# Optimization experiments

Measured on AMD Instinct MI355X. Metric: run time of the kernel, lower is better.

## Reference

```python
import jax, jax.numpy as jnp
import numpy as np

B, C, H, W = 8, 256, 64, 64
DQK = C // 8  # 32
EPS = 1e-5  # BatchNorm eps


def _conv_bn_relu(x, w, b, g, beta, mean, var):
    # 1x1 conv == channel matmul; BN in inference form (running stats)
    y = jnp.einsum('oc,bchw->bohw', w, x) + b[None, :, None, None]
    scale = g / jnp.sqrt(var + EPS)
    y = (y - mean[None, :, None, None]) * scale[None, :, None, None] + beta[None, :, None, None]
    return jax.nn.relu(y)


def setup_inputs() -> dict:
    key = jax.random.key(0)
    ks = jax.random.split(key, 20)
    f32 = jnp.float32

    def rn(i, shape, s=0.05):
        return jax.random.normal(ks[i], shape, dtype=f32) * s

    inp = {
        'x': jax.random.normal(ks[0], (B, C, H, W), dtype=f32),
        # query branch (C -> C//8)
        'wq': rn(1, (DQK, C)), 'bq': rn(2, (DQK,)),
        'gq': 1.0 + rn(3, (DQK,)), 'betaq': rn(4, (DQK,)),
        'mq': rn(5, (DQK,)), 'vq': jnp.abs(1.0 + rn(6, (DQK,))),
        # key branch (C -> C//8)
        'wk': rn(7, (DQK, C)), 'bk': rn(8, (DQK,)),
        'gk': 1.0 + rn(9, (DQK,)), 'betak': rn(10, (DQK,)),
        'mk': rn(11, (DQK,)), 'vk': jnp.abs(1.0 + rn(12, (DQK,))),
        # value branch (C -> C)
        'wv': rn(13, (C, C)), 'bv': rn(14, (C,)),
        'gv': 1.0 + rn(15, (C,)), 'betav': rn(16, (C,)),
        'mv': rn(17, (C,)), 'vv': jnp.abs(1.0 + rn(18, (C,))),
        # learnable residual gate (torch init is 0; nonzero for meaningful grads)
        'gamma': jnp.array([0.5], dtype=f32),
    }
    return inp


def reference(x, wq, bq, gq, betaq, mq, vq,
              wk, bk, gk, betak, mk, vk,
              wv, bv, gv, betav, mv, vv, gamma):
    b, c, h, w = x.shape
    n = h * w
    q = _conv_bn_relu(x, wq, bq, gq, betaq, mq, vq).reshape(b, DQK, n)  # [B,D,N]
    k = _conv_bn_relu(x, wk, bk, gk, betak, mk, vk).reshape(b, DQK, n)  # [B,D,N]
    v = _conv_bn_relu(x, wv, bv, gv, betav, mv, vv).reshape(b, c, n)    # [B,C,N]
    # energy[b,i,j] = <q_i, k_j>, unscaled as in the original
    energy = jnp.einsum('bdi,bdj->bij', q, k)          # [B,N,N]
    attn = jax.nn.softmax(energy, axis=-1)             # softmax over keys j
    # out[b,c,i] = sum_j V[b,c,j] * A[b,i,j]  (bmm with attention^T)
    out = jnp.einsum('bcj,bij->bci', v, attn).reshape(b, c, h, w)
    return gamma.reshape(1, 1, 1, 1) * out + x
```

## Files before the change

### kernel.cpp

```cpp
#include <hip/hip_runtime.h>
#include <math.h>
#include <stdint.h>
#include <stddef.h>

#define NB 8
#define NC 256
#define NN 4096
#define BN_EPS 1e-5f

typedef unsigned short u16;
typedef __attribute__((ext_vector_type(4))) unsigned short u16x4;
typedef __attribute__((ext_vector_type(8))) short bf16x8;
typedef __attribute__((ext_vector_type(4))) float f32x4;

static __device__ __forceinline__ float4 ld4(const float* p) { return *(const float4*)p; }
static __device__ __forceinline__ void st4(float* p, float4 v) { *(float4*)p = v; }
static __device__ __forceinline__ u16 f2bf(float f) {
  uint32_t u = __float_as_uint(f);
  return (u16)((u + 0x7FFFu + ((u >> 16) & 1u)) >> 16);
}

__global__ __launch_bounds__(256) void qkv_fused(
    const float* __restrict__ x,
    const float* __restrict__ wq, const float* __restrict__ bq,
    const float* __restrict__ gq, const float* __restrict__ betaq,
    const float* __restrict__ mq, const float* __restrict__ vq,
    const float* __restrict__ wk, const float* __restrict__ bk,
    const float* __restrict__ gk, const float* __restrict__ betak,
    const float* __restrict__ mk, const float* __restrict__ vk,
    const float* __restrict__ wv, const float* __restrict__ bv,
    const float* __restrict__ gv, const float* __restrict__ betav,
    const float* __restrict__ mv, const float* __restrict__ vv,
    u16* __restrict__ q_bf, u16* __restrict__ k_bf, u16* __restrict__ v_bf)
{
  __shared__ __align__(16) float smem[8704];
  float* sX = smem;
  float* sW = smem + 4096;
  float* sT = smem;

  const int tid   = threadIdx.x;
  const int bx    = blockIdx.x;
  const int b     = bx & 7;
  const int rem   = bx >> 3;
  const int ntile = rem & 31;
  const int otile = rem >> 5;
  const int n0    = ntile * 128;
  const int o0    = otile * 64;

  const int to = tid >> 4;
  const int tn = tid & 15;

  float acc[4][2][4];
#pragma unroll
  for (int j = 0; j < 4; ++j)
#pragma unroll
    for (int r = 0; r < 2; ++r)
#pragma unroll
      for (int e = 0; e < 4; ++e) acc[j][r][e] = 0.f;

  const float* xb = x + (size_t)b * NC * NN + n0;

  for (int ch = 0; ch < 8; ++ch) {
    const int c0 = ch * 32;
#pragma unroll
    for (int p = 0; p < 4; ++p) {
      int f = p * 256 + tid;
      int row = f >> 5, col4 = f & 31;
      st4(sX + row * 128 + col4 * 4, ld4(xb + (size_t)(c0 + row) * NN + col4 * 4));
    }
#pragma unroll
    for (int p = 0; p < 2; ++p) {
      int f = p * 256 + tid;
      int row = f >> 3, col4 = f & 7;
      int o = o0 + row;
      const float* wrow;
      if (o < 32)      wrow = wq + o * NC;
      else if (o < 64) wrow = wk + (o - 32) * NC;
      else             wrow = wv + (o - 64) * NC;
      st4(sW + row * 36 + col4 * 4, ld4(wrow + c0 + col4 * 4));
    }
    __syncthreads();

    for (int cc = 0; cc < 8; ++cc) {
      float wr[4][4];
#pragma unroll
      for (int j = 0; j < 4; ++j) {
        float4 t = ld4(sW + (to * 4 + j) * 36 + cc * 4);
        wr[j][0] = t.x; wr[j][1] = t.y; wr[j][2] = t.z; wr[j][3] = t.w;
      }
      float xr[4][2][4];
#pragma unroll
      for (int lc = 0; lc < 4; ++lc)
#pragma unroll
        for (int r = 0; r < 2; ++r) {
          float4 t = ld4(sX + (cc * 4 + lc) * 128 + tn * 4 + r * 64);
          xr[lc][r][0] = t.x; xr[lc][r][1] = t.y; xr[lc][r][2] = t.z; xr[lc][r][3] = t.w;
        }
#pragma unroll
      for (int j = 0; j < 4; ++j)
#pragma unroll
        for (int lc = 0; lc < 4; ++lc)
#pragma unroll
          for (int r = 0; r < 2; ++r)
#pragma unroll
            for (int e = 0; e < 4; ++e)
              acc[j][r][e] = fmaf(wr[j][lc], xr[lc][r][e], acc[j][r][e]);
    }
    __syncthreads();
  }

  if (otile == 0) {
#pragma unroll
    for (int j = 0; j < 4; ++j) {
      int o = to * 4 + j;
      float bias, g, beta, mean, var;
      if (o < 32) { int d = o;      bias = bq[d]; g = gq[d]; beta = betaq[d]; mean = mq[d]; var = vq[d]; }
      else        { int d = o - 32; bias = bk[d]; g = gk[d]; beta = betak[d]; mean = mk[d]; var = vk[d]; }
      float alpha = g * rsqrtf(var + BN_EPS);
      float delta = (bias - mean) * alpha + beta;
#pragma unroll
      for (int r = 0; r < 2; ++r)
#pragma unroll
        for (int e = 0; e < 4; ++e) {
          float y = fmaxf(fmaf(acc[j][r][e], alpha, delta), 0.f);
          int n = tn * 4 + r * 64 + e;
          sT[n * 68 + to * 4 + j] = y;
        }
    }
    __syncthreads();
    const size_t nrow = (size_t)b * NN + n0;
#pragma unroll
    for (int p = 0; p < 8; ++p) {
      int f = p * 256 + tid;
      int n = f >> 4, col4 = f & 15;
      float4 t = ld4(sT + n * 68 + col4 * 4);
      u16x4 h = { f2bf(t.x), f2bf(t.y), f2bf(t.z), f2bf(t.w) };
      if (col4 < 8) *(u16x4*)(q_bf + (nrow + n) * 32 + col4 * 4) = h;
      else          *(u16x4*)(k_bf + (nrow + n) * 32 + (col4 - 8) * 4) = h;
    }
  } else {
#pragma unroll
    for (int j = 0; j < 4; ++j) {
      int c = (otile - 1) * 64 + to * 4 + j;
      float alpha = gv[c] * rsqrtf(vv[c] + BN_EPS);
      float delta = (bv[c] - mv[c]) * alpha + betav[c];
#pragma unroll
      for (int r = 0; r < 2; ++r) {
        u16x4 h;
#pragma unroll
        for (int e = 0; e < 4; ++e)
          h[e] = f2bf(fmaxf(fmaf(acc[j][r][e], alpha, delta), 0.f));
        int n = n0 + tn * 4 + r * 64;
        *(u16x4*)(v_bf + ((size_t)b * NC + c) * NN + n) = h;
      }
    }
  }
}

__global__ __launch_bounds__(256, 4) void attn_mfma(
    const u16* __restrict__ q_bf, const u16* __restrict__ k_bf,
    const u16* __restrict__ v_bf, const float* __restrict__ x,
    const float* __restrict__ gamma, float* __restrict__ out)
{
  __shared__ u16 sP[4 * 32 * 64];

  const int tid = threadIdx.x;
  const int w   = tid >> 6;
  const int l   = tid & 63;
  const int xl  = l & 15;
  const int g   = l >> 4;
  const int b   = blockIdx.x & 7;
  const int rt  = blockIdx.x >> 3;
  const int i0  = rt * 32;

  u16* sPw = sP + w * 2048;

  const u16* qb = q_bf + ((size_t)b * NN + i0) * 32;
  const u16* kb = k_bf + (size_t)b * NN * 32;
  const u16* vb = v_bf + (size_t)b * NC * NN + (size_t)(w * 64) * NN;

  bf16x8 qf[2];
#pragma unroll
  for (int blk = 0; blk < 2; ++blk)
    qf[blk] = *(const bf16x8*)(qb + (size_t)(blk * 16 + xl) * 32 + 8 * g);

  f32x4 acc[2][4];
#pragma unroll
  for (int blk = 0; blk < 2; ++blk)
#pragma unroll
    for (int ct = 0; ct < 4; ++ct)
      acc[blk][ct] = (f32x4){0.f, 0.f, 0.f, 0.f};

  float mr[2][4], lr[2][4];
#pragma unroll
  for (int blk = 0; blk < 2; ++blk)
#pragma unroll
    for (int r = 0; r < 4; ++r) { mr[blk][r] = -INFINITY; lr[blk][r] = 0.f; }

  for (int jt64 = 0; jt64 < 64; ++jt64) {
    const int j0 = jt64 * 64;

    bf16x8 kf[4];
#pragma unroll
    for (int jb = 0; jb < 4; ++jb)
      kf[jb] = *(const bf16x8*)(kb + (size_t)(j0 + 16 * jb + xl) * 32 + 8 * g);

#pragma unroll
    for (int blk = 0; blk < 2; ++blk) {
      f32x4 s[4];
#pragma unroll
      for (int jb = 0; jb < 4; ++jb)
        s[jb] = __builtin_amdgcn_mfma_f32_16x16x32_bf16(
            qf[blk], kf[jb], (f32x4){0.f, 0.f, 0.f, 0.f}, 0, 0, 0);
      float pm[4];
#pragma unroll
      for (int r = 0; r < 4; ++r)
        pm[r] = fmaxf(fmaxf(s[0][r], s[1][r]), fmaxf(s[2][r], s[3][r]));
#pragma unroll
      for (int msk = 1; msk < 16; msk <<= 1)
#pragma unroll
        for (int r = 0; r < 4; ++r)
          pm[r] = fmaxf(pm[r], __shfl_xor(pm[r], msk));

      bool need = false;
#pragma unroll
      for (int r = 0; r < 4; ++r) need = need || (pm[r] > mr[blk][r]);
      if (__any(need)) {
        float sc[4];
#pragma unroll
        for (int r = 0; r < 4; ++r) {
          float mn = fmaxf(mr[blk][r], pm[r]);
          sc[r] = __expf(mr[blk][r] - mn);
          mr[blk][r] = mn;
          lr[blk][r] *= sc[r];
        }
#pragma unroll
        for (int ct = 0; ct < 4; ++ct)
#pragma unroll
          for (int r = 0; r < 4; ++r) acc[blk][ct][r] *= sc[r];
      }

      float ts[4] = {0.f, 0.f, 0.f, 0.f};
#pragma unroll
      for (int jb = 0; jb < 4; ++jb)
#pragma unroll
        for (int r = 0; r < 4; ++r) {
          float p = __expf(s[jb][r] - mr[blk][r]);
          ts[r] += p;
          int irow = blk * 16 + 4 * g + r;
          sPw[irow * 64 + ((16 * jb + xl) ^ ((irow & 7) << 3))] = f2bf(p);
        }
#pragma unroll
      for (int msk = 1; msk < 16; msk <<= 1)
#pragma unroll
        for (int r = 0; r < 4; ++r) ts[r] += __shfl_xor(ts[r], msk);
#pragma unroll
      for (int r = 0; r < 4; ++r) lr[blk][r] += ts[r];
    }

#pragma unroll
    for (int jt = 0; jt < 2; ++jt) {
      bf16x8 pf[2];
#pragma unroll
      for (int blk = 0; blk < 2; ++blk) {
        int irow = blk * 16 + xl;
        pf[blk] = *(const bf16x8*)(sPw + irow * 64 +
                                   ((jt * 32 + 8 * g) ^ ((irow & 7) << 3)));
      }
#pragma unroll
      for (int ct = 0; ct < 4; ++ct) {
        bf16x8 vf = *(const bf16x8*)(vb + (size_t)(ct * 16 + xl) * NN +
                                     j0 + jt * 32 + 8 * g);
        acc[0][ct] = __builtin_amdgcn_mfma_f32_16x16x32_bf16(pf[0], vf, acc[0][ct], 0, 0, 0);
        acc[1][ct] = __builtin_amdgcn_mfma_f32_16x16x32_bf16(pf[1], vf, acc[1][ct], 0, 0, 0);
      }
    }
  }

  float linv[2][4];
#pragma unroll
  for (int blk = 0; blk < 2; ++blk)
#pragma unroll
    for (int r = 0; r < 4; ++r) linv[blk][r] = 1.f / lr[blk][r];

  const float gm = gamma[0];
#pragma unroll
  for (int blk = 0; blk < 2; ++blk)
#pragma unroll
    for (int ct = 0; ct < 4; ++ct) {
      int c = w * 64 + ct * 16 + xl;
      size_t off = ((size_t)b * NC + c) * NN + i0 + blk * 16 + 4 * g;
      float4 xv = ld4(x + off);
      float4 o4;
      o4.x = fmaf(gm, acc[blk][ct][0] * linv[blk][0], xv.x);
      o4.y = fmaf(gm, acc[blk][ct][1] * linv[blk][1], xv.y);
      o4.z = fmaf(gm, acc[blk][ct][2] * linv[blk][2], xv.z);
      o4.w = fmaf(gm, acc[blk][ct][3] * linv[blk][3], xv.w);
      st4(out + off, o4);
    }
}

extern "C" void kernel_launch(void* const* d_in, const int* in_sizes, int n_in,
                              void* d_out, int out_size, void* d_ws, size_t ws_size,
                              hipStream_t stream) {
  const float* x     = (const float*)d_in[0];
  const float* wq    = (const float*)d_in[1];
  const float* bq    = (const float*)d_in[2];
  const float* gq    = (const float*)d_in[3];
  const float* betaq = (const float*)d_in[4];
  const float* mq    = (const float*)d_in[5];
  const float* vq    = (const float*)d_in[6];
  const float* wk    = (const float*)d_in[7];
  const float* bk    = (const float*)d_in[8];
  const float* gk    = (const float*)d_in[9];
  const float* betak = (const float*)d_in[10];
  const float* mk    = (const float*)d_in[11];
  const float* vk    = (const float*)d_in[12];
  const float* wv    = (const float*)d_in[13];
  const float* bv    = (const float*)d_in[14];
  const float* gv    = (const float*)d_in[15];
  const float* betav = (const float*)d_in[16];
  const float* mv    = (const float*)d_in[17];
  const float* vv    = (const float*)d_in[18];
  const float* gamma = (const float*)d_in[19];
  float* out = (float*)d_out;

  u16* q_bf = (u16*)d_ws;
  u16* k_bf = q_bf + (size_t)NB * NN * 32;
  u16* v_bf = k_bf + (size_t)NB * NN * 32;

  qkv_fused<<<dim3(1280), dim3(256), 0, stream>>>(
      x, wq, bq, gq, betaq, mq, vq,
      wk, bk, gk, betak, mk, vk,
      wv, bv, gv, betav, mv, vv,
      q_bf, k_bf, v_bf);

  attn_mfma<<<dim3(1024), dim3(256), 0, stream>>>(q_bf, k_bf, v_bf, x, gamma, out);
}
```

Measured before the change: 549.4 us.

## Split score and softmax work across waves and share row stats via LDS

Each of the four waves previously recomputed the full 32x64 QK^T tile and its exponentials. Now each wave computes only its own 16-key slice, writes it into a single shared P tile, and exchanges per-row max and sum partials through small LDS arrays, with two block barriers per key tile. Log2(e) is folded into the query BN scale so exp2f replaces __expf. The next key fragment and the V fragments are also loaded earlier to hide latency. In exchange, each iteration gains barrier and LDS traffic, and the last iteration prefetches key data past the end of the batch slice.

New measurement: 627.8 us. 1.14x slower.

```diff
diff --git a/kernel.cpp b/kernel.cpp
--- a/kernel.cpp
+++ b/kernel.cpp
@@ -7,6 +7,7 @@
 #define NC 256
 #define NN 4096
 #define BN_EPS 1e-5f
+#define LOG2E 1.44269504088896340736f
 
 typedef unsigned short u16;
 typedef __attribute__((ext_vector_type(4))) unsigned short u16x4;
@@ -118,6 +119,7 @@
       else        { int d = o - 32; bias = bk[d]; g = gk[d]; beta = betak[d]; mean = mk[d]; var = vk[d]; }
       float alpha = g * rsqrtf(var + BN_EPS);
       float delta = (bias - mean) * alpha + beta;
+      if (o < 32) { alpha *= LOG2E; delta *= LOG2E; }
 #pragma unroll
       for (int r = 0; r < 2; ++r)
 #pragma unroll
@@ -162,7 +164,9 @@
     const u16* __restrict__ v_bf, const float* __restrict__ x,
     const float* __restrict__ gamma, float* __restrict__ out)
 {
-  __shared__ u16 sP[4 * 32 * 64];
+  __shared__ u16 sP[32 * 64];
+  __shared__ float sMx[32 * 4];
+  __shared__ float sLx[32 * 4];
 
   const int tid = threadIdx.x;
   const int w   = tid >> 6;
@@ -173,16 +177,13 @@
   const int rt  = blockIdx.x >> 3;
   const int i0  = rt * 32;
 
-  u16* sPw = sP + w * 2048;
-
-  const u16* qb = q_bf + ((size_t)b * NN + i0) * 32;
-  const u16* kb = k_bf + (size_t)b * NN * 32;
-  const u16* vb = v_bf + (size_t)b * NC * NN + (size_t)(w * 64) * NN;
+  const u16* qb  = q_bf + ((size_t)b * NN + i0) * 32;
+  const u16* kb0 = k_bf + (size_t)b * NN * 32 + (size_t)(16 * w + xl) * 32 + 8 * g;
+  const u16* vb  = v_bf + ((size_t)b * NC + w * 64) * NN;
 
   bf16x8 qf[2];
-#pragma unroll
-  for (int blk = 0; blk < 2; ++blk)
-    qf[blk] = *(const bf16x8*)(qb + (size_t)(blk * 16 + xl) * 32 + 8 * g);
+  qf[0] = *(const bf16x8*)(qb + (size_t)xl * 32 + 8 * g);
+  qf[1] = *(const bf16x8*)(qb + (size_t)(16 + xl) * 32 + 8 * g);
 
   f32x4 acc[2][4];
 #pragma unroll
@@ -197,84 +198,121 @@
 #pragma unroll
     for (int r = 0; r < 4; ++r) { mr[blk][r] = -INFINITY; lr[blk][r] = 0.f; }
 
+  bf16x8 kf = *(const bf16x8*)kb0;
+
   for (int jt64 = 0; jt64 < 64; ++jt64) {
     const int j0 = jt64 * 64;
 
-    bf16x8 kf[4];
-#pragma unroll
-    for (int jb = 0; jb < 4; ++jb)
-      kf[jb] = *(const bf16x8*)(kb + (size_t)(j0 + 16 * jb + xl) * 32 + 8 * g);
-
-#pragma unroll
-    for (int blk = 0; blk < 2; ++blk) {
-      f32x4 s[4];
-#pragma unroll
-      for (int jb = 0; jb < 4; ++jb)
-        s[jb] = __builtin_amdgcn_mfma_f32_16x16x32_bf16(
-            qf[blk], kf[jb], (f32x4){0.f, 0.f, 0.f, 0.f}, 0, 0, 0);
-      float pm[4];
-#pragma unroll
-      for (int r = 0; r < 4; ++r)
-        pm[r] = fmaxf(fmaxf(s[0][r], s[1][r]), fmaxf(s[2][r], s[3][r]));
-#pragma unroll
-      for (int msk = 1; msk < 16; msk <<= 1)
-#pragma unroll
-        for (int r = 0; r < 4; ++r)
-          pm[r] = fmaxf(pm[r], __shfl_xor(pm[r], msk));
-
-      bool need = false;
-#pragma unroll
-      for (int r = 0; r < 4; ++r) need = need || (pm[r] > mr[blk][r]);
-      if (__any(need)) {
-        float sc[4];
-#pragma unroll
-        for (int r = 0; r < 4; ++r) {
-          float mn = fmaxf(mr[blk][r], pm[r]);
-          sc[r] = __expf(mr[blk][r] - mn);
-          mr[blk][r] = mn;
-          lr[blk][r] *= sc[r];
+    f32x4 s0 = __builtin_amdgcn_mfma_f32_16x16x32_bf16(qf[0], kf, (f32x4){0.f,0.f,0.f,0.f}, 0, 0, 0);
+    f32x4 s1 = __builtin_amdgcn_mfma_f32_16x16x32_bf16(qf[1], kf, (f32x4){0.f,0.f,0.f,0.f}, 0, 0, 0);
+
+    bf16x8 kf_next = *(const bf16x8*)(kb0 + (size_t)(j0 + 64) * 32);
+
+    bf16x8 vf[2][4];
+#pragma unroll
+    for (int jt2 = 0; jt2 < 2; ++jt2)
+#pragma unroll
+      for (int ct = 0; ct < 4; ++ct)
+        vf[jt2][ct] = *(const bf16x8*)(vb + (size_t)(ct * 16 + xl) * NN + j0 + jt2 * 32 + 8 * g);
+
+    float q0[4], q1[4];
+#pragma unroll
+    for (int r = 0; r < 4; ++r) { q0[r] = s0[r]; q1[r] = s1[r]; }
+#pragma unroll
+    for (int msk = 1; msk < 16; msk <<= 1) {
+#pragma unroll
+      for (int r = 0; r < 4; ++r) {
+        q0[r] = fmaxf(q0[r], __shfl_xor(q0[r], msk));
+        q1[r] = fmaxf(q1[r], __shfl_xor(q1[r], msk));
+      }
+    }
+    if (xl == 0) {
+#pragma unroll
+      for (int r = 0; r < 4; ++r) {
+        sMx[(4 * g + r) * 4 + w]      = q0[r];
+        sMx[(16 + 4 * g + r) * 4 + w] = q1[r];
+      }
+    }
+    __syncthreads();
+
+    float t0[4], t1[4];
+    bool need = false;
+#pragma unroll
+    for (int r = 0; r < 4; ++r) {
+      float4 m4 = *(const float4*)&sMx[(4 * g + r) * 4];
+      t0[r] = fmaxf(fmaxf(m4.x, m4.y), fmaxf(m4.z, m4.w));
+      need = need || (t0[r] > mr[0][r]);
+      float4 n4 = *(const float4*)&sMx[(16 + 4 * g + r) * 4];
+      t1[r] = fmaxf(fmaxf(n4.x, n4.y), fmaxf(n4.z, n4.w));
+      need = need || (t1[r] > mr[1][r]);
+    }
+    if (__any(need)) {
+#pragma unroll
+      for (int r = 0; r < 4; ++r) {
+        float mn0 = fmaxf(mr[0][r], t0[r]);
+        float sc0 = exp2f(mr[0][r] - mn0);
+        mr[0][r] = mn0; lr[0][r] *= sc0;
+        float mn1 = fmaxf(mr[1][r], t1[r]);
+        float sc1 = exp2f(mr[1][r] - mn1);
+        mr[1][r] = mn1; lr[1][r] *= sc1;
+#pragma unroll
+        for (int ct = 0; ct < 4; ++ct) {
+          acc[0][ct][r] *= sc0;
+          acc[1][ct][r] *= sc1;
         }
-#pragma unroll
-        for (int ct = 0; ct < 4; ++ct)
-#pragma unroll
-          for (int r = 0; r < 4; ++r) acc[blk][ct][r] *= sc[r];
-      }
-
-      float ts[4] = {0.f, 0.f, 0.f, 0.f};
-#pragma unroll
-      for (int jb = 0; jb < 4; ++jb)
-#pragma unroll
-        for (int r = 0; r < 4; ++r) {
-          float p = __expf(s[jb][r] - mr[blk][r]);
-          ts[r] += p;
-          int irow = blk * 16 + 4 * g + r;
-          sPw[irow * 64 + ((16 * jb + xl) ^ ((irow & 7) << 3))] = f2bf(p);
-        }
-#pragma unroll
-      for (int msk = 1; msk < 16; msk <<= 1)
-#pragma unroll
-        for (int r = 0; r < 4; ++r) ts[r] += __shfl_xor(ts[r], msk);
-#pragma unroll
-      for (int r = 0; r < 4; ++r) lr[blk][r] += ts[r];
-    }
-
-#pragma unroll
-    for (int jt = 0; jt < 2; ++jt) {
-      bf16x8 pf[2];
-#pragma unroll
-      for (int blk = 0; blk < 2; ++blk) {
-        int irow = blk * 16 + xl;
-        pf[blk] = *(const bf16x8*)(sPw + irow * 64 +
-                                   ((jt * 32 + 8 * g) ^ ((irow & 7) << 3)));
-      }
+      }
+    }
+
+    float ts0[4], ts1[4];
+#pragma unroll
+    for (int r = 0; r < 4; ++r) {
+      float p0 = exp2f(s0[r] - mr[0][r]);
+      ts0[r] = p0;
+      int row0 = 4 * g + r;
+      sP[row0 * 64 + ((16 * w + xl) ^ ((row0 & 7) << 3))] = f2bf(p0);
+      float p1 = exp2f(s1[r] - mr[1][r]);
+      ts1[r] = p1;
+      int row1 = 16 + 4 * g + r;
+      sP[row1 * 64 + ((16 * w + xl) ^ ((row1 & 7) << 3))] = f2bf(p1);
+    }
+#pragma unroll
+    for (int msk = 1; msk < 16; msk <<= 1) {
+#pragma unroll
+      for (int r = 0; r < 4; ++r) {
+        ts0[r] += __shfl_xor(ts0[r], msk);
+        ts1[r] += __shfl_xor(ts1[r], msk);
+      }
+    }
+    if (xl == 0) {
+#pragma unroll
+      for (int r = 0; r < 4; ++r) {
+        sLx[(4 * g + r) * 4 + w]      = ts0[r];
+        sLx[(16 + 4 * g + r) * 4 + w] = ts1[r];
+      }
+    }
+    __syncthreads();
+
+#pragma unroll
+    for (int r = 0; r < 4; ++r) {
+      float4 l4 = *(const float4*)&sLx[(4 * g + r) * 4];
+      lr[0][r] += (l4.x + l4.y) + (l4.z + l4.w);
+      float4 k4 = *(const float4*)&sLx[(16 + 4 * g + r) * 4];
+      lr[1][r] += (k4.x + k4.y) + (k4.z + k4.w);
+    }
+
+#pragma unroll
+    for (int jt2 = 0; jt2 < 2; ++jt2) {
+      int row0 = xl, row1 = 16 + xl;
+      bf16x8 pf0 = *(const bf16x8*)(sP + row0 * 64 + ((jt2 * 32 + 8 * g) ^ ((row0 & 7) << 3)));
+      bf16x8 pf1 = *(const bf16x8*)(sP + row1 * 64 + ((jt2 * 32 + 8 * g) ^ ((row1 & 7) << 3)));
 #pragma unroll
       for (int ct = 0; ct < 4; ++ct) {
-        bf16x8 vf = *(const bf16x8*)(vb + (size_t)(ct * 16 + xl) * NN +
-                                     j0 + jt * 32 + 8 * g);
-        acc[0][ct] = __builtin_amdgcn_mfma_f32_16x16x32_bf16(pf[0], vf, acc[0][ct], 0, 0, 0);
-        acc[1][ct] = __builtin_amdgcn_mfma_f32_16x16x32_bf16(pf[1], vf, acc[1][ct], 0, 0, 0);
-      }
-    }
+        acc[0][ct] = __builtin_amdgcn_mfma_f32_16x16x32_bf16(pf0, vf[jt2][ct], acc[0][ct], 0, 0, 0);
+        acc[1][ct] = __builtin_amdgcn_mfma_f32_16x16x32_bf16(pf1, vf[jt2][ct], acc[1][ct], 0, 0, 0);
+      }
+    }
+
+    kf = kf_next;
   }
 
   float linv[2][4];
```

## Use exp2 with log2e-prescaled Q, lazy rescale threshold, deferred row-sum reduction

Applied to the files above, without the earlier changes.

Folds log2(e) into the query BN affine so the attention kernel can use exp2f directly. It skips the online-softmax max update unless a new max exceeds the running max by a threshold, and only then does the cross-lane max shuffle. Row sums are kept per lane and reduced once after the loop. P is converted to bf16 by truncation, and V loads are issued earlier and interleaved with the PV MFMAs per row block. The cost targeted is the per-tile shuffle, exp and conversion overhead, traded against possible overflow in the unnormalized accumulators and a small precision loss from truncation.

Measured after the change: 839.4 us. +52.8%, slower.

```diff
diff --git a/kernel.cpp b/kernel.cpp
--- a/kernel.cpp
+++ b/kernel.cpp
@@ -7,6 +7,8 @@
 #define NC 256
 #define NN 4096
 #define BN_EPS 1e-5f
+#define LOG2E 1.44269504088896340736f
+#define THR 24.0f
 
 typedef unsigned short u16;
 typedef __attribute__((ext_vector_type(4))) unsigned short u16x4;
@@ -18,6 +20,9 @@
 static __device__ __forceinline__ u16 f2bf(float f) {
   uint32_t u = __float_as_uint(f);
   return (u16)((u + 0x7FFFu + ((u >> 16) & 1u)) >> 16);
+}
+static __device__ __forceinline__ u16 f2bf_trunc(float f) {
+  return (u16)(__float_as_uint(f) >> 16);
 }
 
 __global__ __launch_bounds__(256) void qkv_fused(
@@ -118,6 +123,7 @@
       else        { int d = o - 32; bias = bk[d]; g = gk[d]; beta = betak[d]; mean = mk[d]; var = vk[d]; }
       float alpha = g * rsqrtf(var + BN_EPS);
       float delta = (bias - mean) * alpha + beta;
+      if (o < 32) { alpha *= LOG2E; delta *= LOG2E; }
 #pragma unroll
       for (int r = 0; r < 2; ++r)
 #pragma unroll
@@ -175,14 +181,13 @@
 
   u16* sPw = sP + w * 2048;
 
-  const u16* qb = q_bf + ((size_t)b * NN + i0) * 32;
-  const u16* kb = k_bf + (size_t)b * NN * 32;
-  const u16* vb = v_bf + (size_t)b * NC * NN + (size_t)(w * 64) * NN;
+  const u16* qb   = q_bf + ((size_t)b * NN + i0) * 32;
+  const u16* kb_l = k_bf + (size_t)b * NN * 32 + (size_t)xl * 32 + 8 * g;
+  const u16* vb_l = v_bf + ((size_t)b * NC + w * 64) * NN + (size_t)xl * NN + 8 * g;
 
   bf16x8 qf[2];
-#pragma unroll
-  for (int blk = 0; blk < 2; ++blk)
-    qf[blk] = *(const bf16x8*)(qb + (size_t)(blk * 16 + xl) * 32 + 8 * g);
+  qf[0] = *(const bf16x8*)(qb + (size_t)xl * 32 + 8 * g);
+  qf[1] = *(const bf16x8*)(qb + (size_t)(16 + xl) * 32 + 8 * g);
 
   f32x4 acc[2][4];
 #pragma unroll
@@ -191,11 +196,11 @@
     for (int ct = 0; ct < 4; ++ct)
       acc[blk][ct] = (f32x4){0.f, 0.f, 0.f, 0.f};
 
-  float mr[2][4], lr[2][4];
+  float mrow[2][4], lsum[2][4];
 #pragma unroll
   for (int blk = 0; blk < 2; ++blk)
 #pragma unroll
-    for (int r = 0; r < 4; ++r) { mr[blk][r] = -INFINITY; lr[blk][r] = 0.f; }
+    for (int r = 0; r < 4; ++r) { mrow[blk][r] = -INFINITY; lsum[blk][r] = 0.f; }
 
   for (int jt64 = 0; jt64 < 64; ++jt64) {
     const int j0 = jt64 * 64;
@@ -203,85 +208,132 @@
     bf16x8 kf[4];
 #pragma unroll
     for (int jb = 0; jb < 4; ++jb)
-      kf[jb] = *(const bf16x8*)(kb + (size_t)(j0 + 16 * jb + xl) * 32 + 8 * g);
-
-#pragma unroll
-    for (int blk = 0; blk < 2; ++blk) {
-      f32x4 s[4];
+      kf[jb] = *(const bf16x8*)(kb_l + (size_t)(j0 + 16 * jb) * 32);
+    bf16x8 vfA[4];
+#pragma unroll
+    for (int ct = 0; ct < 4; ++ct)
+      vfA[ct] = *(const bf16x8*)(vb_l + (size_t)(ct * 16) * NN + j0);
+
+    f32x4 s0[4];
+#pragma unroll
+    for (int jb = 0; jb < 4; ++jb)
+      s0[jb] = __builtin_amdgcn_mfma_f32_16x16x32_bf16(qf[0], kf[jb], (f32x4){0.f,0.f,0.f,0.f}, 0, 0, 0);
+    {
+      float mx[4];
+#pragma unroll
+      for (int r = 0; r < 4; ++r)
+        mx[r] = fmaxf(fmaxf(s0[0][r], s0[1][r]), fmaxf(s0[2][r], s0[3][r]));
+      bool need = false;
+#pragma unroll
+      for (int r = 0; r < 4; ++r) need = need || (mx[r] > mrow[0][r] + THR);
+      if (__any(need)) {
+#pragma unroll
+        for (int msk = 1; msk < 16; msk <<= 1)
+#pragma unroll
+          for (int r = 0; r < 4; ++r) mx[r] = fmaxf(mx[r], __shfl_xor(mx[r], msk));
+#pragma unroll
+        for (int r = 0; r < 4; ++r) {
+          float mn = fmaxf(mrow[0][r], mx[r]);
+          float sc = exp2f(mrow[0][r] - mn);
+          mrow[0][r] = mn; lsum[0][r] *= sc;
+#pragma unroll
+          for (int ct = 0; ct < 4; ++ct) acc[0][ct][r] *= sc;
+        }
+      }
 #pragma unroll
       for (int jb = 0; jb < 4; ++jb)
-        s[jb] = __builtin_amdgcn_mfma_f32_16x16x32_bf16(
-            qf[blk], kf[jb], (f32x4){0.f, 0.f, 0.f, 0.f}, 0, 0, 0);
-      float pm[4];
+#pragma unroll
+        for (int r = 0; r < 4; ++r) {
+          float p = exp2f(s0[jb][r] - mrow[0][r]);
+          lsum[0][r] += p;
+          int row = 4 * g + r;
+          sPw[row * 64 + ((16 * jb + xl) ^ ((row & 7) << 3))] = f2bf_trunc(p);
+        }
+    }
+    {
+      int row = xl;
+      bf16x8 pf = *(const bf16x8*)(sPw + row * 64 + ((8 * g) ^ ((row & 7) << 3)));
+#pragma unroll
+      for (int ct = 0; ct < 4; ++ct)
+        acc[0][ct] = __builtin_amdgcn_mfma_f32_16x16x32_bf16(pf, vfA[ct], acc[0][ct], 0, 0, 0);
+    }
+
+    f32x4 s1[4];
+#pragma unroll
+    for (int jb = 0; jb < 4; ++jb)
+      s1[jb] = __builtin_amdgcn_mfma_f32_16x16x32_bf16(qf[1], kf[jb], (f32x4){0.f,0.f,0.f,0.f}, 0, 0, 0);
+    bf16x8 vfB[4];
+#pragma unroll
+    for (int ct = 0; ct < 4; ++ct)
+      vfB[ct] = *(const bf16x8*)(vb_l + (size_t)(ct * 16) * NN + j0 + 32);
+    {
+      float mx[4];
 #pragma unroll
       for (int r = 0; r < 4; ++r)
-        pm[r] = fmaxf(fmaxf(s[0][r], s[1][r]), fmaxf(s[2][r], s[3][r]));
-#pragma unroll
-      for (int msk = 1; msk < 16; msk <<= 1)
-#pragma unroll
-        for (int r = 0; r < 4; ++r)
-          pm[r] = fmaxf(pm[r], __shfl_xor(pm[r], msk));
-
+        mx[r] = fmaxf(fmaxf(s1[0][r], s1[1][r]), fmaxf(s1[2][r], s1[3][r]));
       bool need = false;
 #pragma unroll
-      for (int r = 0; r < 4; ++r) need = need || (pm[r] > mr[blk][r]);
+      for (int r = 0; r < 4; ++r) need = need || (mx[r] > mrow[1][r] + THR);
       if (__any(need)) {
-        float sc[4];
+#pragma unroll
+        for (int msk = 1; msk < 16; msk <<= 1)
+#pragma unroll
+          for (int r = 0; r < 4; ++r) mx[r] = fmaxf(mx[r], __shfl_xor(mx[r], msk));
 #pragma unroll
         for (int r = 0; r < 4; ++r) {
-          float mn = fmaxf(mr[blk][r], pm[r]);
-          sc[r] = __expf(mr[blk][r] - mn);
-          mr[blk][r] = mn;
-          lr[blk][r] *= sc[r];
-        }
-#pragma unroll
-        for (int ct = 0; ct < 4; ++ct)
-#pragma unroll
-          for (int r = 0; r < 4; ++r) acc[blk][ct][r] *= sc[r];
+          float mn = fmaxf(mrow[1][r], mx[r]);
+          float sc = exp2f(mrow[1][r] - mn);
+          mrow[1][r] = mn; lsum[1][r] *= sc;
+#pragma unroll
+          for (int ct = 0; ct < 4; ++ct) acc[1][ct][r] *= sc;
+        }
       }
-
-      float ts[4] = {0.f, 0.f, 0.f, 0.f};
 #pragma unroll
       for (int jb = 0; jb < 4; ++jb)
 #pragma unroll
         for (int r = 0; r < 4; ++r) {
-          float p = __expf(s[jb][r] - mr[blk][r]);
-          ts[r] += p;
-          int irow = blk * 16 + 4 * g + r;
-          sPw[irow * 64 + ((16 * jb + xl) ^ ((irow & 7) << 3))] = f2bf(p);
-        }
-#pragma unroll
-      for (int msk = 1; msk < 16; msk <<= 1)
-#pragma unroll
-        for (int r = 0; r < 4; ++r) ts[r] += __shfl_xor(ts[r], msk);
-#pragma unroll
-      for (int r = 0; r < 4; ++r) lr[blk][r] += ts[r];
-    }
-
-#pragma unroll
-    for (int jt = 0; jt < 2; ++jt) {
-      bf16x8 pf[2];
-#pragma unroll
-      for (int blk = 0; blk < 2; ++blk) {
-        int irow = blk * 16 + xl;
-        pf[blk] = *(const bf16x8*)(sPw + irow * 64 +
-                                   ((jt * 32 + 8 * g) ^ ((irow & 7) << 3)));
-      }
-#pragma unroll
-      for (int ct = 0; ct < 4; ++ct) {
-        bf16x8 vf = *(const bf16x8*)(vb + (size_t)(ct * 16 + xl) * NN +
-                                     j0 + jt * 32 + 8 * g);
-        acc[0][ct] = __builtin_amdgcn_mfma_f32_16x16x32_bf16(pf[0], vf, acc[0][ct], 0, 0, 0);
-        acc[1][ct] = __builtin_amdgcn_mfma_f32_16x16x32_bf16(pf[1], vf, acc[1][ct], 0, 0, 0);
-      }
+          float p = exp2f(s1[jb][r] - mrow[1][r]);
+          lsum[1][r] += p;
+          int row = 16 + 4 * g + r;
+          sPw[row * 64 + ((16 * jb + xl) ^ ((row & 7) << 3))] = f2bf_trunc(p);
+        }
+    }
+    {
+      int row = 16 + xl;
+      bf16x8 pf = *(const bf16x8*)(sPw + row * 64 + ((8 * g) ^ ((row & 7) << 3)));
+#pragma unroll
+      for (int ct = 0; ct < 4; ++ct)
+        acc[1][ct] = __builtin_amdgcn_mfma_f32_16x16x32_bf16(pf, vfA[ct], acc[1][ct], 0, 0, 0);
+    }
+    {
+      int row = xl;
+      bf16x8 pf = *(const bf16x8*)(sPw + row * 64 + ((32 + 8 * g) ^ ((row & 7) << 3)));
+#pragma unroll
+      for (int ct = 0; ct < 4; ++ct)
+        acc[0][ct] = __builtin_amdgcn_mfma_f32_16x16x32_bf16(pf, vfB[ct], acc[0][ct], 0, 0, 0);
+    }
+    {
+      int row = 16 + xl;
+      bf16x8 pf = *(const bf16x8*)(sPw + row * 64 + ((32 + 8 * g) ^ ((row & 7) << 3)));
+#pragma unroll
+      for (int ct = 0; ct < 4; ++ct)
+        acc[1][ct] = __builtin_amdgcn_mfma_f32_16x16x32_bf16(pf, vfB[ct], acc[1][ct], 0, 0, 0);
     }
   }
 
+#pragma unroll
+  for (int msk = 1; msk < 16; msk <<= 1)
+#pragma unroll
+    for (int blk = 0; blk < 2; ++blk)
+#pragma unroll
+      for (int r = 0; r < 4; ++r)
+        lsum[blk][r] += __shfl_xor(lsum[blk][r], msk);
+
   float linv[2][4];
 #pragma unroll
   for (int blk = 0; blk < 2; ++blk)
 #pragma unroll
-    for (int r = 0; r < 4; ++r) linv[blk][r] = 1.f / lr[blk][r];
+    for (int r = 0; r < 4; ++r) linv[blk][r] = 1.f / lsum[blk][r];
 
   const float gm = gamma[0];
 #pragma unroll
```
